# Kernel tuning notes

Hardware: AMD Instinct MI355X
Metric: run time of the kernel (lower is better)

Reference implementation:

```python
import jax, jax.numpy as jnp
import numpy as np

N_NODES = 100000
N_EDGES = 1250000
IN_CH = 128
OUT_CH = 64


def setup_inputs() -> dict:
    key = jax.random.key(0)
    k1, k2, k3, k4 = jax.random.split(key, 4)
    x = jax.random.normal(k1, (N_NODES, IN_CH), dtype=jnp.float32)
    edge_index = jax.random.randint(k2, (2, N_EDGES), 0, N_NODES, dtype=jnp.int64)
    edge_weight = jax.random.uniform(k3, (N_EDGES,), dtype=jnp.float32)
    # Xavier-uniform weight, zero bias (as in reset_parameters)
    limit = float(np.sqrt(6.0 / (IN_CH + OUT_CH)))
    W = jax.random.uniform(k4, (IN_CH, OUT_CH), dtype=jnp.float32, minval=-limit, maxval=limit)
    b = jnp.zeros((OUT_CH,), dtype=jnp.float32)
    return {"x": x, "edge_index": edge_index, "edge_weight": edge_weight, "W": W, "b": b}


def reference(x, edge_index, edge_weight, W, b):
    # Dense transform: [N, in] @ [in, out] -> [N, out]
    h = jnp.matmul(x, W)
    row, col = edge_index[0], edge_index[1]
    n = h.shape[0]
    # Weighted in-degree via scatter-add on destination (row)
    deg = jnp.zeros((n,), dtype=h.dtype).at[row].add(edge_weight)
    # deg^-0.5 with inf (deg==0) replaced by 0
    deg_inv_sqrt = jnp.where(deg == 0, jnp.zeros_like(deg), deg ** -0.5)
    norm = deg_inv_sqrt[row] * deg_inv_sqrt[col]  # [E]
    # Gather source features, normalize, scatter-add to destinations
    out = jnp.zeros_like(h).at[row].add(h[col] * norm[:, None])
    return out + b
```

## Files before the change

kernel.cpp:

```cpp
#include <hip/hip_runtime.h>

#define N_NODES 100000
#define N_EDGES 1250000
#define IN_CH 128
#define OUT_CH 64

#define NPB 128
#define ACCS2 33
#define NBINS 782
#define BINCAP_DEF 2048
#define NB1 256
#define B1T 512
#define CH1 ((N_EDGES + NB1 - 1) / NB1)
#define MAXU ((CH1 + B1T - 1) / B1T)
#define CURS_STRIDE 16
#define GEMM_BLOCKS ((N_NODES + 127) / 128)

#define QSCALE 8192.0f
#define QBIAS_F 8388608.0f
#define QBIAS_U 8388608u
#define INV_QSCALE 1.220703125e-4f
#define SCALE_DEG 33554432.0f
#define INV_SCALE_DEG 2.9802322387695312e-08f

typedef __attribute__((ext_vector_type(8))) short short8;
typedef __attribute__((ext_vector_type(4))) float f32x4;

__device__ inline unsigned int f2bf(float f) {
    unsigned int u = __float_as_uint(f);
    unsigned int r = ((u >> 16) & 1u) + 0x7FFFu;
    return (u + r) >> 16;
}
__device__ inline float bf_lo(unsigned int p) { return __uint_as_float(p << 16); }
__device__ inline float bf_hi(unsigned int p) { return __uint_as_float(p & 0xFFFF0000u); }

__device__ inline unsigned long long qpacks(unsigned int p, float sc) {
    unsigned int lo = (unsigned int)__float2int_rn(fmaf(bf_lo(p), sc, QBIAS_F));
    unsigned int hi = (unsigned int)__float2int_rn(fmaf(bf_hi(p), sc, QBIAS_F));
    return ((unsigned long long)hi << 32) | (unsigned long long)lo;
}

__global__ __launch_bounds__(256) void init_kernel(const float* __restrict__ W,
                                                   unsigned int* __restrict__ Wb,
                                                   int* __restrict__ cursor,
                                                   int bincap) {
    int g = blockIdx.x * 256 + threadIdx.x;
    if (g < NBINS) cursor[g * CURS_STRIDE] = g * bincap;

    int c = g >> 8;
    int t4 = (g >> 6) & 3;
    int l = g & 63;
    int q = l >> 4, r15 = l & 15;
    unsigned int o[4];
#pragma unroll
    for (int jj = 0; jj < 4; ++jj) {
        float f0 = W[(c * 32 + q * 8 + 2 * jj)     * OUT_CH + t4 * 16 + r15];
        float f1 = W[(c * 32 + q * 8 + 2 * jj + 1) * OUT_CH + t4 * 16 + r15];
        o[jj] = f2bf(f0) | (f2bf(f1) << 16);
    }
    *(uint4*)(Wb + (size_t)g * 4) = make_uint4(o[0], o[1], o[2], o[3]);
}

__global__ __launch_bounds__(512) void fused_kernel(const float* __restrict__ x,
                                                    const unsigned int* __restrict__ Wb,
                                                    const int* __restrict__ ei,
                                                    const float* __restrict__ ew,
                                                    int* __restrict__ cursor,
                                                    int2* __restrict__ brec,
                                                    unsigned int* __restrict__ hs,
                                                    int bincap) {
    __shared__ int hist[NBINS];
    __shared__ int base[NBINS];
    __shared__ int rank[NBINS];
    const int tid = threadIdx.x;

    if (blockIdx.x < NB1) {
        for (int i = tid; i < NBINS; i += B1T) { hist[i] = 0; rank[i] = 0; }
        __syncthreads();

        const int e0 = blockIdx.x * CH1;
        const int e1 = (e0 + CH1 < N_EDGES) ? e0 + CH1 : N_EDGES;

        int rowv[MAXU], colv[MAXU];
        float wv[MAXU];
#pragma unroll
        for (int u = 0; u < MAXU; ++u) {
            int e = e0 + tid + u * B1T;
            bool ok = e < e1;
            rowv[u] = ok ? ei[e] : -1;
            colv[u] = ok ? ei[N_EDGES + e] : 0;
            wv[u]   = ok ? ew[e] : 0.0f;
            if (ok) atomicAdd(&hist[rowv[u] >> 7], 1);
        }
        __syncthreads();

        for (int i = tid; i < NBINS; i += B1T)
            if (hist[i] > 0) base[i] = atomicAdd(&cursor[i * CURS_STRIDE], hist[i]);
        __syncthreads();

#pragma unroll
        for (int u = 0; u < MAXU; ++u) {
            if (rowv[u] >= 0) {
                int bb = rowv[u] >> 7;
                int rk = atomicAdd(&rank[bb], 1);
                int idx = base[bb] + rk;
                if (idx < (bb + 1) * bincap)
                    brec[idx] = make_int2(((rowv[u] & 127) << 17) | colv[u],
                                          __float_as_int(wv[u]));
            }
        }
    } else {
        const int blk  = blockIdx.x - NB1;
        const int w    = tid >> 6;
        const int lane = tid & 63;
        const int q    = lane >> 4, r15 = lane & 15;
        const int node = blk * 128 + w * 16 + r15;
        const int nl   = (node < N_NODES) ? node : N_NODES - 1;
        const float* xrow = x + (size_t)nl * IN_CH;

        f32x4 acc[4];
#pragma unroll
        for (int t = 0; t < 4; ++t) acc[t] = (f32x4){0.f, 0.f, 0.f, 0.f};

#pragma unroll
        for (int c = 0; c < 4; ++c) {
            float4 xa = *(const float4*)(xrow + c * 32 + q * 8);
            float4 xb = *(const float4*)(xrow + c * 32 + q * 8 + 4);
            short8 bfrag;
            bfrag[0] = (short)f2bf(xa.x); bfrag[1] = (short)f2bf(xa.y);
            bfrag[2] = (short)f2bf(xa.z); bfrag[3] = (short)f2bf(xa.w);
            bfrag[4] = (short)f2bf(xb.x); bfrag[5] = (short)f2bf(xb.y);
            bfrag[6] = (short)f2bf(xb.z); bfrag[7] = (short)f2bf(xb.w);
#pragma unroll
            for (int t = 0; t < 4; ++t) {
                short8 afrag = *(const short8*)(Wb + (size_t)((c * 4 + t) * 64 + lane) * 4);
                acc[t] = __builtin_amdgcn_mfma_f32_16x16x32_bf16(afrag, bfrag, acc[t], 0, 0, 0);
            }
        }

        if (node < N_NODES) {
#pragma unroll
            for (int t = 0; t < 4; ++t) {
                unsigned int p0 = f2bf(acc[t][0]) | (f2bf(acc[t][1]) << 16);
                unsigned int p1 = f2bf(acc[t][2]) | (f2bf(acc[t][3]) << 16);
                *(uint2*)(hs + (size_t)node * 32 + t * 8 + q * 2) = make_uint2(p0, p1);
            }
        }
    }
}

__global__ __launch_bounds__(256) void bin2_kernel(const int* __restrict__ cursor,
                                                   const int2* __restrict__ brec,
                                                   float* __restrict__ dis_g,
                                                   int bincap) {
    __shared__ int deg[NPB];
    const int t = threadIdx.x;
    const int b = blockIdx.x;
    if (t < NPB) deg[t] = 0;
    __syncthreads();

    const int rbase = b * bincap;
    int m = cursor[b * CURS_STRIDE] - rbase;
    if (m > bincap) m = bincap;

    for (int j = t; j < m; j += 256) {
        int2 rec = brec[rbase + j];
        atomicAdd(&deg[rec.x >> 17], __float2int_rn(__int_as_float(rec.y) * SCALE_DEG));
    }
    __syncthreads();

    int node = b * NPB + t;
    if (t < NPB && node < N_NODES) {
        float d = (float)deg[t] * INV_SCALE_DEG;
        dis_g[node] = (d == 0.0f) ? 0.0f : (1.0f / sqrtf(d));
    }
}

__global__ __launch_bounds__(512) void gather_kernel(const int* __restrict__ cursor,
                                                     const int2* __restrict__ brec,
                                                     const uint4* __restrict__ hs,
                                                     const float* __restrict__ dis,
                                                     const float* __restrict__ b,
                                                     float* __restrict__ out,
                                                     int bincap) {
    __shared__ unsigned long long acc[NPB * ACCS2];
    __shared__ int cnt[NPB];
    const int tid = threadIdx.x;
    const int blk = blockIdx.x;
    for (int k = tid; k < NPB * ACCS2; k += 512) acc[k] = 0ull;
    if (tid < NPB) cnt[tid] = 0;
    __syncthreads();

    const int rbase = blk * bincap;
    int m = cursor[blk * CURS_STRIDE] - rbase;
    if (m > bincap) m = bincap;

    const int wid = tid >> 6, lane = tid & 63;
    const int sub = lane >> 3, l8 = lane & 7;

    for (int j0 = wid * 16; j0 < m; j0 += 128) {
        int jA = j0 + sub;
        int jB = j0 + 8 + sub;
        bool okA = jA < m, okB = jB < m;
        int recA = okA ? brec[rbase + jA].x : 0;
        int recB = okB ? brec[rbase + jB].x : 0;
        uint4 pA = make_uint4(0, 0, 0, 0), pB = make_uint4(0, 0, 0, 0);
        if (okA) pA = hs[(size_t)(recA & 0x1FFFF) * 8 + l8];
        if (okB) pB = hs[(size_t)(recB & 0x1FFFF) * 8 + l8];
        if (okA) {
            float sc = QSCALE * dis[recA & 0x1FFFF];
            int ba = (recA >> 17) * ACCS2 + 4 * l8;
            atomicAdd(&acc[ba + 0], qpacks(pA.x, sc));
            atomicAdd(&acc[ba + 1], qpacks(pA.y, sc));
            atomicAdd(&acc[ba + 2], qpacks(pA.z, sc));
            atomicAdd(&acc[ba + 3], qpacks(pA.w, sc));
            if (l8 == 0) atomicAdd(&cnt[recA >> 17], 1);
        }
        if (okB) {
            float sc = QSCALE * dis[recB & 0x1FFFF];
            int bb = (recB >> 17) * ACCS2 + 4 * l8;
            atomicAdd(&acc[bb + 0], qpacks(pB.x, sc));
            atomicAdd(&acc[bb + 1], qpacks(pB.y, sc));
            atomicAdd(&acc[bb + 2], qpacks(pB.z, sc));
            atomicAdd(&acc[bb + 3], qpacks(pB.w, sc));
            if (l8 == 0) atomicAdd(&cnt[recB >> 17], 1);
        }
    }
    __syncthreads();

    const unsigned int* acc32 = (const unsigned int*)acc;
    float bc = b[lane];
    int half = lane & 1, slot = lane >> 1;
#pragma unroll 4
    for (int r = 0; r < 16; ++r) {
        int nl = wid * 16 + r;
        int node = blk * NPB + nl;
        if (node < N_NODES) {
            unsigned int raw = acc32[(nl * ACCS2 + slot) * 2 + half];
            int qsum = (int)(raw - (unsigned int)cnt[nl] * QBIAS_U);
            float di = dis[node] * INV_QSCALE;
            out[(size_t)node * OUT_CH + lane] = (float)qsum * di + bc;
        }
    }
}

extern "C" void kernel_launch(void* const* d_in, const int* in_sizes, int n_in,
                              void* d_out, int out_size, void* d_ws, size_t ws_size,
                              hipStream_t stream) {
    const float* x  = (const float*)d_in[0];
    const int*   ei = (const int*)d_in[1];
    const float* ew = (const float*)d_in[2];
    const float* W  = (const float*)d_in[3];
    const float* b  = (const float*)d_in[4];
    float* out = (float*)d_out;

    unsigned int* hs = (unsigned int*)d_ws;
    unsigned int* Wb = hs + (size_t)N_NODES * 32;
    int*   cursor  = (int*)(Wb + 4096);
    float* dis     = (float*)(cursor + NBINS * CURS_STRIDE);
    int2*  brec    = (int2*)(dis + N_NODES);
    size_t used = (size_t)N_NODES * 32 + 4096 + (size_t)NBINS * CURS_STRIDE
                + (size_t)N_NODES;
    size_t rem  = (ws_size / 4 > used) ? ws_size / 4 - used : 0;
    int bincap  = (int)(rem / (2 * (size_t)NBINS));
    if (bincap > BINCAP_DEF) bincap = BINCAP_DEF;

    init_kernel<<<4, 256, 0, stream>>>(W, Wb, cursor, bincap);
    fused_kernel<<<NB1 + GEMM_BLOCKS, 512, 0, stream>>>(x, Wb, ei, ew, cursor,
                                                        brec, hs, bincap);
    bin2_kernel<<<NBINS, 256, 0, stream>>>(cursor, brec, dis, bincap);
    gather_kernel<<<NBINS, 512, 0, stream>>>(cursor, brec, (const uint4*)hs,
                                             dis, b, out, bincap);
}
```

Baseline: 164.9 us.

## Replace atomic bin cursors with histogram, prefix scan and separate scatter pass

Binning now builds a per-block histogram that is written to global memory. A per-bin scan kernel computes deterministic offsets, and a separate scatter kernel writes the edge records, replacing the global atomic cursor allocation. The gather loop also processes four records per iteration instead of two, so more hs loads are in flight. In exchange, edge_index is read twice and two extra kernel launches are added.

```diff
diff --git a/kernel.cpp b/kernel.cpp
--- a/kernel.cpp
+++ b/kernel.cpp
@@ -8,12 +8,12 @@
 #define NPB 128
 #define ACCS2 33
 #define NBINS 782
+#define HPAD 784
 #define BINCAP_DEF 2048
 #define NB1 256
 #define B1T 512
 #define CH1 ((N_EDGES + NB1 - 1) / NB1)
 #define MAXU ((CH1 + B1T - 1) / B1T)
-#define CURS_STRIDE 16
 #define GEMM_BLOCKS ((N_NODES + 127) / 128)
 
 #define QSCALE 8192.0f
@@ -41,12 +41,8 @@
 }
 
 __global__ __launch_bounds__(256) void init_kernel(const float* __restrict__ W,
-                                                   unsigned int* __restrict__ Wb,
-                                                   int* __restrict__ cursor,
-                                                   int bincap) {
+                                                   unsigned int* __restrict__ Wb) {
     int g = blockIdx.x * 256 + threadIdx.x;
-    if (g < NBINS) cursor[g * CURS_STRIDE] = g * bincap;
-
     int c = g >> 8;
     int t4 = (g >> 6) & 3;
     int l = g & 63;
@@ -64,51 +60,26 @@
 __global__ __launch_bounds__(512) void fused_kernel(const float* __restrict__ x,
                                                     const unsigned int* __restrict__ Wb,
                                                     const int* __restrict__ ei,
-                                                    const float* __restrict__ ew,
-                                                    int* __restrict__ cursor,
-                                                    int2* __restrict__ brec,
-                                                    unsigned int* __restrict__ hs,
-                                                    int bincap) {
+                                                    int* __restrict__ hist2d,
+                                                    unsigned int* __restrict__ hs) {
     __shared__ int hist[NBINS];
-    __shared__ int base[NBINS];
-    __shared__ int rank[NBINS];
     const int tid = threadIdx.x;
 
     if (blockIdx.x < NB1) {
-        for (int i = tid; i < NBINS; i += B1T) { hist[i] = 0; rank[i] = 0; }
+        for (int i = tid; i < NBINS; i += B1T) hist[i] = 0;
         __syncthreads();
 
         const int e0 = blockIdx.x * CH1;
         const int e1 = (e0 + CH1 < N_EDGES) ? e0 + CH1 : N_EDGES;
-
-        int rowv[MAXU], colv[MAXU];
-        float wv[MAXU];
 #pragma unroll
         for (int u = 0; u < MAXU; ++u) {
             int e = e0 + tid + u * B1T;
-            bool ok = e < e1;
-            rowv[u] = ok ? ei[e] : -1;
-            colv[u] = ok ? ei[N_EDGES + e] : 0;
-            wv[u]   = ok ? ew[e] : 0.0f;
-            if (ok) atomicAdd(&hist[rowv[u] >> 7], 1);
+            if (e < e1) atomicAdd(&hist[ei[e] >> 7], 1);
         }
         __syncthreads();
 
-        for (int i = tid; i < NBINS; i += B1T)
-            if (hist[i] > 0) base[i] = atomicAdd(&cursor[i * CURS_STRIDE], hist[i]);
-        __syncthreads();
-
-#pragma unroll
-        for (int u = 0; u < MAXU; ++u) {
-            if (rowv[u] >= 0) {
-                int bb = rowv[u] >> 7;
-                int rk = atomicAdd(&rank[bb], 1);
-                int idx = base[bb] + rk;
-                if (idx < (bb + 1) * bincap)
-                    brec[idx] = make_int2(((rowv[u] & 127) << 17) | colv[u],
-                                          __float_as_int(wv[u]));
-            }
-        }
+        int* hrow = hist2d + blockIdx.x * HPAD;
+        for (int i = tid; i < NBINS; i += B1T) hrow[i] = hist[i];
     } else {
         const int blk  = blockIdx.x - NB1;
         const int w    = tid >> 6;
@@ -149,7 +120,61 @@
     }
 }
 
-__global__ __launch_bounds__(256) void bin2_kernel(const int* __restrict__ cursor,
+__global__ __launch_bounds__(256) void scan_kernel(const int* __restrict__ hist2d,
+                                                   int* __restrict__ offs2d,
+                                                   int* __restrict__ mtot,
+                                                   int bincap) {
+    __shared__ int tmp[256];
+    const int b = blockIdx.x, t = threadIdx.x;
+    int v = hist2d[t * HPAD + b];
+    int acc = v;
+    tmp[t] = acc;
+    __syncthreads();
+#pragma unroll
+    for (int d = 1; d < 256; d <<= 1) {
+        int add = (t >= d) ? tmp[t - d] : 0;
+        __syncthreads();
+        acc += add;
+        tmp[t] = acc;
+        __syncthreads();
+    }
+    offs2d[b * 256 + t] = b * bincap + (acc - v);
+    if (t == 255) mtot[b] = acc;
+}
+
+__global__ __launch_bounds__(B1T) void scatter_kernel(const int* __restrict__ ei,
+                                                      const float* __restrict__ ew,
+                                                      const int* __restrict__ offs2d,
+                                                      int2* __restrict__ brec,
+                                                      int bincap) {
+    __shared__ int rank[NBINS];
+    __shared__ int base[NBINS];
+    const int t = threadIdx.x;
+    for (int i = t; i < NBINS; i += B1T) {
+        rank[i] = 0;
+        base[i] = offs2d[i * 256 + blockIdx.x];
+    }
+    __syncthreads();
+
+    const int e0 = blockIdx.x * CH1;
+    const int e1 = (e0 + CH1 < N_EDGES) ? e0 + CH1 : N_EDGES;
+#pragma unroll
+    for (int u = 0; u < MAXU; ++u) {
+        int e = e0 + t + u * B1T;
+        if (e < e1) {
+            int row = ei[e];
+            int col = ei[N_EDGES + e];
+            float w = ew[e];
+            int bb = row >> 7;
+            int rk = atomicAdd(&rank[bb], 1);
+            int idx = base[bb] + rk;
+            if (idx < (bb + 1) * bincap)
+                brec[idx] = make_int2(((row & 127) << 17) | col, __float_as_int(w));
+        }
+    }
+}
+
+__global__ __launch_bounds__(256) void bin2_kernel(const int* __restrict__ mtot,
                                                    const int2* __restrict__ brec,
                                                    float* __restrict__ dis_g,
                                                    int bincap) {
@@ -160,7 +185,7 @@
     __syncthreads();
 
     const int rbase = b * bincap;
-    int m = cursor[b * CURS_STRIDE] - rbase;
+    int m = mtot[b];
     if (m > bincap) m = bincap;
 
     for (int j = t; j < m; j += 256) {
@@ -176,7 +201,7 @@
     }
 }
 
-__global__ __launch_bounds__(512) void gather_kernel(const int* __restrict__ cursor,
+__global__ __launch_bounds__(512) void gather_kernel(const int* __restrict__ mtot,
                                                      const int2* __restrict__ brec,
                                                      const uint4* __restrict__ hs,
                                                      const float* __restrict__ dis,
@@ -192,38 +217,39 @@
     __syncthreads();
 
     const int rbase = blk * bincap;
-    int m = cursor[blk * CURS_STRIDE] - rbase;
+    int m = mtot[blk];
     if (m > bincap) m = bincap;
 
     const int wid = tid >> 6, lane = tid & 63;
     const int sub = lane >> 3, l8 = lane & 7;
 
-    for (int j0 = wid * 16; j0 < m; j0 += 128) {
-        int jA = j0 + sub;
-        int jB = j0 + 8 + sub;
-        bool okA = jA < m, okB = jB < m;
-        int recA = okA ? brec[rbase + jA].x : 0;
-        int recB = okB ? brec[rbase + jB].x : 0;
-        uint4 pA = make_uint4(0, 0, 0, 0), pB = make_uint4(0, 0, 0, 0);
-        if (okA) pA = hs[(size_t)(recA & 0x1FFFF) * 8 + l8];
-        if (okB) pB = hs[(size_t)(recB & 0x1FFFF) * 8 + l8];
-        if (okA) {
-            float sc = QSCALE * dis[recA & 0x1FFFF];
-            int ba = (recA >> 17) * ACCS2 + 4 * l8;
-            atomicAdd(&acc[ba + 0], qpacks(pA.x, sc));
-            atomicAdd(&acc[ba + 1], qpacks(pA.y, sc));
-            atomicAdd(&acc[ba + 2], qpacks(pA.z, sc));
-            atomicAdd(&acc[ba + 3], qpacks(pA.w, sc));
-            if (l8 == 0) atomicAdd(&cnt[recA >> 17], 1);
-        }
-        if (okB) {
-            float sc = QSCALE * dis[recB & 0x1FFFF];
-            int bb = (recB >> 17) * ACCS2 + 4 * l8;
-            atomicAdd(&acc[bb + 0], qpacks(pB.x, sc));
-            atomicAdd(&acc[bb + 1], qpacks(pB.y, sc));
-            atomicAdd(&acc[bb + 2], qpacks(pB.z, sc));
-            atomicAdd(&acc[bb + 3], qpacks(pB.w, sc));
-            if (l8 == 0) atomicAdd(&cnt[recB >> 17], 1);
+    for (int j0 = wid * 32; j0 < m; j0 += 256) {
+        bool ok[4];
+        int rec[4];
+        uint4 p[4];
+        float sc[4];
+#pragma unroll
+        for (int s = 0; s < 4; ++s) {
+            int jj = j0 + 8 * s + sub;
+            ok[s] = jj < m;
+            rec[s] = ok[s] ? brec[rbase + jj].x : 0;
+        }
+#pragma unroll
+        for (int s = 0; s < 4; ++s) {
+            p[s] = ok[s] ? hs[(size_t)(rec[s] & 0x1FFFF) * 8 + l8]
+                         : make_uint4(0, 0, 0, 0);
+            sc[s] = ok[s] ? QSCALE * dis[rec[s] & 0x1FFFF] : 0.0f;
+        }
+#pragma unroll
+        for (int s = 0; s < 4; ++s) {
+            if (ok[s]) {
+                int ba = (rec[s] >> 17) * ACCS2 + 4 * l8;
+                atomicAdd(&acc[ba + 0], qpacks(p[s].x, sc[s]));
+                atomicAdd(&acc[ba + 1], qpacks(p[s].y, sc[s]));
+                atomicAdd(&acc[ba + 2], qpacks(p[s].z, sc[s]));
+                atomicAdd(&acc[ba + 3], qpacks(p[s].w, sc[s]));
+                if (l8 == 0) atomicAdd(&cnt[rec[s] >> 17], 1);
+            }
         }
     }
     __syncthreads();
@@ -256,19 +282,22 @@
 
     unsigned int* hs = (unsigned int*)d_ws;
     unsigned int* Wb = hs + (size_t)N_NODES * 32;
-    int*   cursor  = (int*)(Wb + 4096);
-    float* dis     = (float*)(cursor + NBINS * CURS_STRIDE);
-    int2*  brec    = (int2*)(dis + N_NODES);
-    size_t used = (size_t)N_NODES * 32 + 4096 + (size_t)NBINS * CURS_STRIDE
-                + (size_t)N_NODES;
+    int* hist2d = (int*)(Wb + 4096);
+    int* offs2d = hist2d + NB1 * HPAD;
+    int* mtot   = offs2d + NBINS * 256;
+    float* dis  = (float*)(mtot + 800);
+    int2* brec  = (int2*)(dis + N_NODES);
+    size_t used = (size_t)N_NODES * 32 + 4096 + (size_t)NB1 * HPAD
+                + (size_t)NBINS * 256 + 800 + (size_t)N_NODES;
     size_t rem  = (ws_size / 4 > used) ? ws_size / 4 - used : 0;
     int bincap  = (int)(rem / (2 * (size_t)NBINS));
     if (bincap > BINCAP_DEF) bincap = BINCAP_DEF;
 
-    init_kernel<<<4, 256, 0, stream>>>(W, Wb, cursor, bincap);
-    fused_kernel<<<NB1 + GEMM_BLOCKS, 512, 0, stream>>>(x, Wb, ei, ew, cursor,
-                                                        brec, hs, bincap);
-    bin2_kernel<<<NBINS, 256, 0, stream>>>(cursor, brec, dis, bincap);
-    gather_kernel<<<NBINS, 512, 0, stream>>>(cursor, brec, (const uint4*)hs,
+    init_kernel<<<4, 256, 0, stream>>>(W, Wb);
+    fused_kernel<<<NB1 + GEMM_BLOCKS, 512, 0, stream>>>(x, Wb, ei, hist2d, hs);
+    scan_kernel<<<NBINS, 256, 0, stream>>>(hist2d, offs2d, mtot, bincap);
+    scatter_kernel<<<NB1, B1T, 0, stream>>>(ei, ew, offs2d, brec, bincap);
+    bin2_kernel<<<NBINS, 256, 0, stream>>>(mtot, brec, dis, bincap);
+    gather_kernel<<<NBINS, 512, 0, stream>>>(mtot, brec, (const uint4*)hs,
                                              dis, b, out, bincap);
 }
```

Result: slower. 171.9 us (+4.2%).
